# Kernel optimization log

Hardware: AMD Instinct MI355X
Metric: run time of the kernel (lower is better)

## Reference

```python
import jax, jax.numpy as jnp
import numpy as np

EMBED = 1024
NUM_EXPERTS = 8
TOP_K = 2


def setup_inputs() -> dict:
    key = jax.random.key(0)
    ks = jax.random.split(key, 6)
    scale = EMBED ** -0.5  # keep activations numerically sane
    return {
        "x": jax.random.normal(ks[0], (4, 4096, EMBED), jnp.float32),
        "router_w": jax.random.normal(ks[1], (EMBED, NUM_EXPERTS), jnp.float32) * scale,
        "router_b": jnp.zeros((NUM_EXPERTS,), jnp.float32),
        "we_gate": jax.random.normal(ks[2], (NUM_EXPERTS, EMBED, EMBED), jnp.float32) * scale,
        "we_up": jax.random.normal(ks[3], (NUM_EXPERTS, EMBED, EMBED), jnp.float32) * scale,
        "we_down": jax.random.normal(ks[4], (NUM_EXPERTS, EMBED, EMBED), jnp.float32) * scale,
    }


def reference(x, router_w, router_b, we_gate, we_up, we_down):
    x_shape = x.shape
    x_flat = x.reshape(-1, x_shape[-1])            # [T, D]
    num_tokens = x_flat.shape[0]

    router_logits = x_flat @ router_w + router_b    # [T, E]
    topk_weights, topk_indices = jax.lax.top_k(router_logits, k=TOP_K)
    topk_weights = jax.nn.softmax(topk_weights, axis=-1)  # [T, K]

    token_idx_mesh = jnp.repeat(jnp.arange(num_tokens), TOP_K)  # [T*K]
    expert_idx_mesh = topk_indices.reshape(-1)                  # [T*K]

    sort_permutation = jnp.argsort(expert_idx_mesh)  # stable sort by expert
    sorted_expert_idx = expert_idx_mesh[sort_permutation]
    sorted_token_idx = token_idx_mesh[sort_permutation]
    group_sizes = jnp.bincount(sorted_expert_idx, length=NUM_EXPERTS)

    sorted_tokens = x_flat[sorted_token_idx]  # [T*K, D] gather (ragged dispatch)

    ff_gate = jax.lax.ragged_dot(sorted_tokens, we_gate, group_sizes)  # [T*K, D]
    ff_up = jax.lax.ragged_dot(sorted_tokens, we_up, group_sizes)      # [T*K, D]
    activated = jax.nn.silu(ff_gate) * ff_up
    ff_out = jax.lax.ragged_dot(activated, we_down, group_sizes)       # [T*K, D]

    # fuse router weighting into the combine (scatter-add) step
    sorted_weights = topk_weights.reshape(-1)[sort_permutation]  # [T*K]
    ff_out = ff_out * sorted_weights[:, None]

    output_flat = jnp.zeros_like(x_flat).at[sorted_token_idx].add(ff_out)
    return output_flat.reshape(x_shape)
```

## Files before the change

### kernel.cpp

```cpp
#include <hip/hip_runtime.h>
#include <hip/hip_bf16.h>
#include <cstdint>
#include <cstddef>

typedef unsigned short u16;
typedef unsigned int u32;
typedef __attribute__((ext_vector_type(8))) short short8;
typedef __attribute__((ext_vector_type(4))) float floatx4;

#define DD 1024
#define NE 8

#define GLOAD_LDS16(G, L)                                               \
  __builtin_amdgcn_global_load_lds(                                     \
      (const __attribute__((address_space(1))) void*)(G),               \
      (__attribute__((address_space(3))) void*)(L), 16, 0, 0)

__device__ __forceinline__ u16 f2bf(float f) {
  union { __hip_bfloat16 h; u16 u; } cv;
  cv.h = __float2bfloat16(f);
  return cv.u;
}

__device__ __forceinline__ float2 bf2f2(u32 u) {
  union { u32 v; float f; } lo, hi;
  lo.v = u << 16; hi.v = u & 0xffff0000u;
  float2 r; r.x = lo.f; r.y = hi.f; return r;
}

__global__ __launch_bounds__(256) void router_kernel(
    const float* __restrict__ x, const float* __restrict__ rw,
    const float* __restrict__ rb, int2* __restrict__ experts,
    float2* __restrict__ wts, u16* __restrict__ xbf, int T) {
  const int wave = threadIdx.x >> 6;
  const int lane = threadIdx.x & 63;
  const int t = blockIdx.x * 4 + wave;
  if (t >= T) return;
  const float* xr = x + (size_t)t * DD;
  float acc[NE] = {0.f, 0.f, 0.f, 0.f, 0.f, 0.f, 0.f, 0.f};
#pragma unroll
  for (int i = 0; i < 16; i++) {
    const int idx = lane + i * 64;
    const float xv = xr[idx];
    xbf[(size_t)t * DD + idx] = f2bf(xv);
    const float4* r4 = (const float4*)(rw + (size_t)idx * NE);
    float4 a = r4[0], b = r4[1];
    acc[0] += xv * a.x; acc[1] += xv * a.y; acc[2] += xv * a.z; acc[3] += xv * a.w;
    acc[4] += xv * b.x; acc[5] += xv * b.y; acc[6] += xv * b.z; acc[7] += xv * b.w;
  }
#pragma unroll
  for (int s = 1; s < 64; s <<= 1)
#pragma unroll
    for (int e = 0; e < NE; e++)
      acc[e] += __shfl_xor(acc[e], s);
  if (lane == 0) {
    float lg[NE];
#pragma unroll
    for (int e = 0; e < NE; e++) lg[e] = acc[e] + rb[e];
    float l0 = lg[0]; int i0 = 0;
#pragma unroll
    for (int e = 1; e < NE; e++) if (lg[e] > l0) { l0 = lg[e]; i0 = e; }
    float l1 = -3.4e38f; int i1 = 0;
#pragma unroll
    for (int e = 0; e < NE; e++) {
      if (e == i0) continue;
      if (lg[e] > l1) { l1 = lg[e]; i1 = e; }
    }
    const float w0 = 1.f / (1.f + expf(l1 - l0));
    experts[t] = make_int2(i0, i1);
    wts[t] = make_float2(w0, 1.f - w0);
  }
}

__global__ __launch_bounds__(256) void count_kernel(
    const int2* __restrict__ experts, int* __restrict__ counts, int T) {
  __shared__ int lc[NE];
  if (threadIdx.x < NE) lc[threadIdx.x] = 0;
  __syncthreads();
  const int t = blockIdx.x * 256 + threadIdx.x;
  if (t < T) {
    int2 e = experts[t];
    atomicAdd(&lc[e.x], 1);
    atomicAdd(&lc[e.y], 1);
  }
  __syncthreads();
  if (threadIdx.x < NE && lc[threadIdx.x] > 0)
    atomicAdd(&counts[threadIdx.x], lc[threadIdx.x]);
}

__global__ void offsets_kernel(const int* __restrict__ counts, int* __restrict__ offsets) {
  int s = 0;
  for (int e = 0; e < NE; e++) { offsets[e] = s; s += counts[e]; }
}

__global__ __launch_bounds__(256) void scatter_kernel(
    const int2* __restrict__ experts, const int* __restrict__ offsets,
    int* __restrict__ cursors, int* __restrict__ tok_id,
    int2* __restrict__ slots, int T) {
  __shared__ int lc[NE], lb[NE];
  if (threadIdx.x < NE) lc[threadIdx.x] = 0;
  __syncthreads();
  const int t = blockIdx.x * 256 + threadIdx.x;
  int2 e = make_int2(0, 0);
  int p0 = 0, p1 = 0;
  if (t < T) {
    e = experts[t];
    p0 = atomicAdd(&lc[e.x], 1);
    p1 = atomicAdd(&lc[e.y], 1);
  }
  __syncthreads();
  if (threadIdx.x < NE) lb[threadIdx.x] = atomicAdd(&cursors[threadIdx.x], lc[threadIdx.x]);
  __syncthreads();
  if (t < T) {
    const int s0 = offsets[e.x] + lb[e.x] + p0;
    const int s1 = offsets[e.y] + lb[e.y] + p1;
    tok_id[s0] = t;
    tok_id[s1] = t;
    slots[t] = make_int2(s0, s1);
  }
}

__global__ __launch_bounds__(256) void convert_kernel(
    const float* __restrict__ wg, const float* __restrict__ wu,
    const float* __restrict__ wd, u16* __restrict__ Wgu, u16* __restrict__ Wd) {
  const int z = blockIdx.z;
  const int mat = z >> 3;
  const int e = z & 7;
  const float* src = (mat == 0 ? wg : (mat == 1 ? wu : wd)) + (size_t)e * DD * DD;
  __shared__ float tile[64][65];
  const int k0 = blockIdx.y * 64, n0 = blockIdx.x * 64;
  const int tx = threadIdx.x & 63, ty = threadIdx.x >> 6;
#pragma unroll
  for (int i = 0; i < 16; i++) {
    const int kk = i * 4 + ty;
    tile[kk][tx] = src[(size_t)(k0 + kk) * DD + n0 + tx];
  }
  __syncthreads();
#pragma unroll
  for (int i = 0; i < 16; i++) {
    const int nn = i * 4 + ty;
    const int n = n0 + nn;
    const u16 h = f2bf(tile[tx][nn]);
    if (mat == 2) {
      Wd[((size_t)e * DD + n) * DD + k0 + tx] = h;
    } else {
      const int nc = ((n >> 3) << 4) | (mat << 3) | (n & 7);
      Wgu[((size_t)e * 2048 + nc) * DD + k0 + tx] = h;
    }
  }
}

__global__ __launch_bounds__(256) void gateup_kernel(
    const u16* __restrict__ xbf, const u16* __restrict__ Wgu,
    const int* __restrict__ tok_id, const int* __restrict__ offsets,
    const int* __restrict__ counts, u16* __restrict__ H) {
  const int e = blockIdx.z;
  const int cnt = counts[e];
  const int m0 = blockIdx.y * 128;
  if (m0 >= cnt) return;
  const int off = offsets[e];
  const int n0 = blockIdx.x * 128;

  __shared__ u16 As[128 * 64];
  __shared__ u16 Bs[128 * 64];

  const int t = threadIdx.x;
  const int lane = t & 63;
  const int wave = t >> 6;
  const int wm = (wave >> 1) * 64;
  const int wn = (wave & 1) * 64;
  const int r16 = lane & 15;
  const int quad = lane >> 4;

  const int drow = t >> 3;
  const int dpos = t & 7;
  const u16* srcA[4];
  const u16* srcB[4];
  const u16* bbase = Wgu + ((size_t)e * 2048 + n0) * DD;
#pragma unroll
  for (int i = 0; i < 4; i++) {
    const int row = drow + i * 32;
    int r = m0 + row; if (r > cnt - 1) r = cnt - 1;
    const int tok = tok_id[off + r];
    const int ka = (dpos ^ (row & 7)) * 8;
    srcA[i] = xbf + (size_t)tok * DD + ka;
    srcB[i] = bbase + (size_t)row * DD + ka;
  }

  floatx4 acc[4][4];
#pragma unroll
  for (int i = 0; i < 4; i++)
#pragma unroll
    for (int j = 0; j < 4; j++)
      acc[i][j] = (floatx4){0.f, 0.f, 0.f, 0.f};

#pragma unroll 1
  for (int k0 = 0; k0 < DD; k0 += 64) {
    __syncthreads();
#pragma unroll
    for (int i = 0; i < 4; i++) {
      GLOAD_LDS16(srcA[i] + k0, &As[t * 8 + i * 2048]);
      GLOAD_LDS16(srcB[i] + k0, &Bs[t * 8 + i * 2048]);
    }
    __syncthreads();
#pragma unroll
    for (int s = 0; s < 2; s++) {
      short8 a[4], b[4];
#pragma unroll
      for (int i = 0; i < 4; i++)
        a[i] = *(const short8*)&As[(wm + i * 16 + r16) * 64 + (((s << 2) + quad) ^ (r16 & 7)) * 8];
#pragma unroll
      for (int j = 0; j < 4; j++)
        b[j] = *(const short8*)&Bs[(wn + j * 16 + r16) * 64 + (((s << 2) + quad) ^ (r16 & 7)) * 8];
#pragma unroll
      for (int i = 0; i < 4; i++)
#pragma unroll
        for (int j = 0; j < 4; j++)
          acc[i][j] = __builtin_amdgcn_mfma_f32_16x16x32_bf16(a[i], b[j], acc[i][j], 0, 0, 0);
    }
  }

#pragma unroll
  for (int i = 0; i < 4; i++) {
    const int mb = m0 + wm + i * 16 + quad * 4;
#pragma unroll
    for (int j = 0; j < 4; j++) {
      const int nc = n0 + wn + j * 16 + r16;
      const int ng = ((nc >> 4) << 3) | (nc & 7);
#pragma unroll
      for (int r = 0; r < 4; r++) {
        const float v = acc[i][j][r];
        const float pv = __shfl_xor(v, 8);
        const float g = (lane & 8) ? pv : v;
        const float u = (lane & 8) ? v : pv;
        const float hv = g * u / (1.f + __expf(-g));
        const int m = mb + r;
        if (!(lane & 8) && m < cnt)
          H[(size_t)(off + m) * DD + ng] = f2bf(hv);
      }
    }
  }
}

__global__ __launch_bounds__(256) void down_kernel(
    const u16* __restrict__ H, const u16* __restrict__ Wd,
    const int* __restrict__ counts, const int* __restrict__ offsets,
    u16* __restrict__ Y, int TK2) {
  const int e = blockIdx.z;
  const int cnt = counts[e];
  const int m0 = blockIdx.y * 128;
  if (m0 >= cnt) return;
  const int off = offsets[e];
  const int n0 = blockIdx.x * 128;

  __shared__ u16 As[128 * 64];
  __shared__ u16 Bs[128 * 64];

  const int t = threadIdx.x;
  const int lane = t & 63;
  const int wave = t >> 6;
  const int wm = (wave >> 1) * 64;
  const int wn = (wave & 1) * 64;
  const int r16 = lane & 15;
  const int quad = lane >> 4;

  const int drow = t >> 3;
  const int dpos = t & 7;
  const u16* srcA[4];
  const u16* srcB[4];
  const u16* bbase = Wd + ((size_t)e * DD + n0) * DD;
#pragma unroll
  for (int i = 0; i < 4; i++) {
    const int row = drow + i * 32;
    int r = off + m0 + row; if (r > TK2 - 1) r = TK2 - 1;
    const int ka = (dpos ^ (row & 7)) * 8;
    srcA[i] = H + (size_t)r * DD + ka;
    srcB[i] = bbase + (size_t)row * DD + ka;
  }

  floatx4 acc[4][4];
#pragma unroll
  for (int i = 0; i < 4; i++)
#pragma unroll
    for (int j = 0; j < 4; j++)
      acc[i][j] = (floatx4){0.f, 0.f, 0.f, 0.f};

#pragma unroll 1
  for (int k0 = 0; k0 < DD; k0 += 64) {
    __syncthreads();
#pragma unroll
    for (int i = 0; i < 4; i++) {
      GLOAD_LDS16(srcA[i] + k0, &As[t * 8 + i * 2048]);
      GLOAD_LDS16(srcB[i] + k0, &Bs[t * 8 + i * 2048]);
    }
    __syncthreads();
#pragma unroll
    for (int s = 0; s < 2; s++) {
      short8 a[4], b[4];
#pragma unroll
      for (int i = 0; i < 4; i++)
        a[i] = *(const short8*)&As[(wm + i * 16 + r16) * 64 + (((s << 2) + quad) ^ (r16 & 7)) * 8];
#pragma unroll
      for (int j = 0; j < 4; j++)
        b[j] = *(const short8*)&Bs[(wn + j * 16 + r16) * 64 + (((s << 2) + quad) ^ (r16 & 7)) * 8];
#pragma unroll
      for (int i = 0; i < 4; i++)
#pragma unroll
        for (int j = 0; j < 4; j++)
          acc[i][j] = __builtin_amdgcn_mfma_f32_16x16x32_bf16(a[i], b[j], acc[i][j], 0, 0, 0);
    }
  }

#pragma unroll
  for (int i = 0; i < 4; i++) {
    const int mb = m0 + wm + i * 16 + quad * 4;
#pragma unroll
    for (int r = 0; r < 4; r++) {
      const int m = mb + r;
      if (m < cnt) {
        u16* yrow = Y + (size_t)(off + m) * DD + n0 + wn + r16;
#pragma unroll
        for (int j = 0; j < 4; j++)
          yrow[j * 16] = f2bf(acc[i][j][r]);
      }
    }
  }
}

__global__ __launch_bounds__(256) void combine_kernel(
    const u16* __restrict__ Y, const int2* __restrict__ slots,
    const float2* __restrict__ wts, float* __restrict__ out, int T) {
  const int wave = threadIdx.x >> 6;
  const int lane = threadIdx.x & 63;
  const int t = blockIdx.x * 4 + wave;
  if (t >= T) return;
  const int2 s = slots[t];
  const float2 w = wts[t];
  const uint4* y0 = (const uint4*)(Y + (size_t)s.x * DD);
  const uint4* y1 = (const uint4*)(Y + (size_t)s.y * DD);
  float4* o = (float4*)(out + (size_t)t * DD);
#pragma unroll
  for (int c = 0; c < 2; c++) {
    const int idx = lane + c * 64;
    const uint4 a = y0[idx];
    const uint4 b = y1[idx];
    const u32 au[4] = {a.x, a.y, a.z, a.w};
    const u32 bu[4] = {b.x, b.y, b.z, b.w};
    float4 r[2];
#pragma unroll
    for (int q = 0; q < 4; q++) {
      const float2 fa = bf2f2(au[q]);
      const float2 fb = bf2f2(bu[q]);
      ((float*)r)[q * 2]     = w.x * fa.x + w.y * fb.x;
      ((float*)r)[q * 2 + 1] = w.x * fa.y + w.y * fb.y;
    }
    o[idx * 2]     = r[0];
    o[idx * 2 + 1] = r[1];
  }
}

extern "C" void kernel_launch(void* const* d_in, const int* in_sizes, int n_in,
                              void* d_out, int out_size, void* d_ws, size_t ws_size,
                              hipStream_t stream) {
  const float* x  = (const float*)d_in[0];
  const float* rw = (const float*)d_in[1];
  const float* rb = (const float*)d_in[2];
  const float* wg = (const float*)d_in[3];
  const float* wu = (const float*)d_in[4];
  const float* wd = (const float*)d_in[5];
  float* out = (float*)d_out;
  const int T = in_sizes[0] / DD;
  const int TK2 = 2 * T;

  char* p = (char*)d_ws;
  int* ctrl = (int*)p; p += 256;
  int2* experts = (int2*)p;  p += (size_t)T * 8;
  float2* wtsp  = (float2*)p; p += (size_t)T * 8;
  int* tok_id   = (int*)p;   p += (size_t)TK2 * 4;
  int2* slots   = (int2*)p;  p += (size_t)T * 8;
  u16* Wd       = (u16*)p;   p += (size_t)NE * DD * DD * 2;
  u16* H        = (u16*)p;   p += (size_t)TK2 * DD * 2;
  u16* Wgu      = (u16*)p;
  u16* xbf      = (u16*)(p + (size_t)NE * 2048 * DD * 2);
  u16* Y        = (u16*)p;
  p += (size_t)TK2 * DD * 2;
  if ((size_t)(p - (char*)d_ws) > ws_size) return;

  hipMemsetAsync(ctrl, 0, 256, stream);

  router_kernel<<<T / 4, 256, 0, stream>>>(x, rw, rb, experts, wtsp, xbf, T);
  count_kernel<<<T / 256, 256, 0, stream>>>(experts, ctrl, T);
  offsets_kernel<<<1, 1, 0, stream>>>(ctrl, ctrl + 16);
  scatter_kernel<<<T / 256, 256, 0, stream>>>(experts, ctrl + 16, ctrl + 8, tok_id, slots, T);
  convert_kernel<<<dim3(16, 16, 24), 256, 0, stream>>>(wg, wu, wd, Wgu, Wd);
  gateup_kernel<<<dim3(16, (T + 127) / 128, NE), 256, 0, stream>>>(
      xbf, Wgu, tok_id, ctrl + 16, ctrl, H);
  down_kernel<<<dim3(8, (T + 127) / 128, NE), 256, 0, stream>>>(
      H, Wd, ctrl, ctrl + 16, Y, TK2);
  combine_kernel<<<T / 4, 256, 0, stream>>>(Y, slots, wtsp, out, T);
}
```

Before: 517.5 us.

## Use 256x256 tiles with 4-stage async LDS pipeline in expert GEMMs

Both expert GEMM kernels move from 128x128 tiles with 256 threads and a single-buffered K=64 loop to 256x256 tiles with 512 threads. They now use a 4-deep ring of K=32 LDS buffers filled by direct global-to-LDS loads, gated with explicit vmcnt waits and raw barriers. MFMA sections are wrapped in s_setprio, and the LDS swizzle is reworked for the 32-wide rows. The aim is to overlap global loads with MFMA work and raise arithmetic intensity per block. The cost is 128 KB of LDS per block, 128 accumulator registers per lane, and more wasted work on ragged expert tails.

Measured after the change: 587.9 us. 13.6% more time.

```diff
diff --git a/kernel.cpp b/kernel.cpp
--- a/kernel.cpp
+++ b/kernel.cpp
@@ -150,78 +150,105 @@
   }
 }
 
-__global__ __launch_bounds__(256) void gateup_kernel(
+
+#define GEMM256_LOOP()                                                  \
+  STAGE(0); STAGE(1); STAGE(2);                                         \
+  asm volatile("s_waitcnt vmcnt(8)" ::: "memory");                      \
+  __builtin_amdgcn_s_barrier();                                         \
+  asm volatile("" ::: "memory");                                        \
+  _Pragma("unroll 1")                                                   \
+  for (int kt = 0; kt < 29; ++kt) {                                     \
+    STAGE((kt + 3) & 3);                                                \
+    COMPUTE((kt & 3) * 8192);                                           \
+    asm volatile("s_waitcnt vmcnt(8)" ::: "memory");                    \
+    __builtin_amdgcn_s_barrier();                                       \
+    asm volatile("" ::: "memory");                                      \
+  }                                                                     \
+  COMPUTE(1 * 8192);                                                    \
+  asm volatile("s_waitcnt vmcnt(4)" ::: "memory");                      \
+  __builtin_amdgcn_s_barrier();                                         \
+  asm volatile("" ::: "memory");                                        \
+  COMPUTE(2 * 8192);                                                    \
+  asm volatile("s_waitcnt vmcnt(0)" ::: "memory");                      \
+  __builtin_amdgcn_s_barrier();                                         \
+  asm volatile("" ::: "memory");                                        \
+  COMPUTE(3 * 8192);
+
+#define STAGE(BUF)                                                      \
+  {                                                                     \
+    GLOAD_LDS16(sA0, &As[(BUF) * 8192 + t * 8]);                        \
+    GLOAD_LDS16(sA1, &As[(BUF) * 8192 + 4096 + t * 8]);                 \
+    GLOAD_LDS16(sB0, &Bs[(BUF) * 8192 + t * 8]);                        \
+    GLOAD_LDS16(sB1, &Bs[(BUF) * 8192 + 4096 + t * 8]);                 \
+    sA0 += 32; sA1 += 32; sB0 += 32; sB1 += 32;                         \
+  }
+
+#define COMPUTE(BUFO)                                                   \
+  {                                                                     \
+    short8 a[8], b[4];                                                  \
+    _Pragma("unroll")                                                   \
+    for (int i = 0; i < 8; i++)                                         \
+      a[i] = *(const short8*)&As[(BUFO) + offA + i * 512];              \
+    _Pragma("unroll")                                                   \
+    for (int j = 0; j < 4; j++)                                         \
+      b[j] = *(const short8*)&Bs[(BUFO) + offB + j * 512];              \
+    __builtin_amdgcn_s_setprio(1);                                      \
+    _Pragma("unroll")                                                   \
+    for (int i = 0; i < 8; i++)                                         \
+      _Pragma("unroll")                                                 \
+      for (int j = 0; j < 4; j++)                                       \
+        acc[i][j] = __builtin_amdgcn_mfma_f32_16x16x32_bf16(            \
+            a[i], b[j], acc[i][j], 0, 0, 0);                            \
+    __builtin_amdgcn_s_setprio(0);                                      \
+  }
+
+__global__ __launch_bounds__(512, 2) void gateup_kernel(
     const u16* __restrict__ xbf, const u16* __restrict__ Wgu,
     const int* __restrict__ tok_id, const int* __restrict__ offsets,
     const int* __restrict__ counts, u16* __restrict__ H) {
   const int e = blockIdx.z;
   const int cnt = counts[e];
-  const int m0 = blockIdx.y * 128;
+  const int m0 = blockIdx.y * 256;
   if (m0 >= cnt) return;
   const int off = offsets[e];
-  const int n0 = blockIdx.x * 128;
-
-  __shared__ u16 As[128 * 64];
-  __shared__ u16 Bs[128 * 64];
+  const int n0 = blockIdx.x * 256;
+
+  __shared__ u16 As[4 * 8192];
+  __shared__ u16 Bs[4 * 8192];
 
   const int t = threadIdx.x;
   const int lane = t & 63;
   const int wave = t >> 6;
-  const int wm = (wave >> 1) * 64;
-  const int wn = (wave & 1) * 64;
+  const int wm = (wave >> 2) * 128;
+  const int wn = (wave & 3) * 64;
   const int r16 = lane & 15;
   const int quad = lane >> 4;
-
-  const int drow = t >> 3;
-  const int dpos = t & 7;
-  const u16* srcA[4];
-  const u16* srcB[4];
-  const u16* bbase = Wgu + ((size_t)e * 2048 + n0) * DD;
-#pragma unroll
-  for (int i = 0; i < 4; i++) {
-    const int row = drow + i * 32;
-    int r = m0 + row; if (r > cnt - 1) r = cnt - 1;
-    const int tok = tok_id[off + r];
-    const int ka = (dpos ^ (row & 7)) * 8;
-    srcA[i] = xbf + (size_t)tok * DD + ka;
-    srcB[i] = bbase + (size_t)row * DD + ka;
-  }
-
-  floatx4 acc[4][4];
-#pragma unroll
-  for (int i = 0; i < 4; i++)
+  const int swz = quad ^ ((r16 >> 1) & 3);
+  const int offA = (wm + r16) * 32 + swz * 8;
+  const int offB = (wn + r16) * 32 + swz * 8;
+
+  const int drow = t >> 2;
+  const int dpos = t & 3;
+  const int c8 = (dpos ^ ((drow >> 1) & 3)) * 8;
+  int r0 = m0 + drow;       if (r0 > cnt - 1) r0 = cnt - 1;
+  int r1 = m0 + drow + 128; if (r1 > cnt - 1) r1 = cnt - 1;
+  const u16* sA0 = xbf + (size_t)tok_id[off + r0] * DD + c8;
+  const u16* sA1 = xbf + (size_t)tok_id[off + r1] * DD + c8;
+  const u16* bbase = Wgu + ((size_t)e * 2048 + n0) * DD + c8;
+  const u16* sB0 = bbase + (size_t)drow * DD;
+  const u16* sB1 = bbase + (size_t)(drow + 128) * DD;
+
+  floatx4 acc[8][4];
+#pragma unroll
+  for (int i = 0; i < 8; i++)
 #pragma unroll
     for (int j = 0; j < 4; j++)
       acc[i][j] = (floatx4){0.f, 0.f, 0.f, 0.f};
 
-#pragma unroll 1
-  for (int k0 = 0; k0 < DD; k0 += 64) {
-    __syncthreads();
-#pragma unroll
-    for (int i = 0; i < 4; i++) {
-      GLOAD_LDS16(srcA[i] + k0, &As[t * 8 + i * 2048]);
-      GLOAD_LDS16(srcB[i] + k0, &Bs[t * 8 + i * 2048]);
-    }
-    __syncthreads();
-#pragma unroll
-    for (int s = 0; s < 2; s++) {
-      short8 a[4], b[4];
-#pragma unroll
-      for (int i = 0; i < 4; i++)
-        a[i] = *(const short8*)&As[(wm + i * 16 + r16) * 64 + (((s << 2) + quad) ^ (r16 & 7)) * 8];
-#pragma unroll
-      for (int j = 0; j < 4; j++)
-        b[j] = *(const short8*)&Bs[(wn + j * 16 + r16) * 64 + (((s << 2) + quad) ^ (r16 & 7)) * 8];
-#pragma unroll
-      for (int i = 0; i < 4; i++)
-#pragma unroll
-        for (int j = 0; j < 4; j++)
-          acc[i][j] = __builtin_amdgcn_mfma_f32_16x16x32_bf16(a[i], b[j], acc[i][j], 0, 0, 0);
-    }
-  }
-
-#pragma unroll
-  for (int i = 0; i < 4; i++) {
+  GEMM256_LOOP();
+
+#pragma unroll
+  for (int i = 0; i < 8; i++) {
     const int mb = m0 + wm + i * 16 + quad * 4;
 #pragma unroll
     for (int j = 0; j < 4; j++) {
@@ -242,77 +269,53 @@
   }
 }
 
-__global__ __launch_bounds__(256) void down_kernel(
+__global__ __launch_bounds__(512, 2) void down_kernel(
     const u16* __restrict__ H, const u16* __restrict__ Wd,
     const int* __restrict__ counts, const int* __restrict__ offsets,
     u16* __restrict__ Y, int TK2) {
   const int e = blockIdx.z;
   const int cnt = counts[e];
-  const int m0 = blockIdx.y * 128;
+  const int m0 = blockIdx.y * 256;
   if (m0 >= cnt) return;
   const int off = offsets[e];
-  const int n0 = blockIdx.x * 128;
-
-  __shared__ u16 As[128 * 64];
-  __shared__ u16 Bs[128 * 64];
+  const int n0 = blockIdx.x * 256;
+
+  __shared__ u16 As[4 * 8192];
+  __shared__ u16 Bs[4 * 8192];
 
   const int t = threadIdx.x;
   const int lane = t & 63;
   const int wave = t >> 6;
-  const int wm = (wave >> 1) * 64;
-  const int wn = (wave & 1) * 64;
+  const int wm = (wave >> 2) * 128;
+  const int wn = (wave & 3) * 64;
   const int r16 = lane & 15;
   const int quad = lane >> 4;
-
-  const int drow = t >> 3;
-  const int dpos = t & 7;
-  const u16* srcA[4];
-  const u16* srcB[4];
-  const u16* bbase = Wd + ((size_t)e * DD + n0) * DD;
-#pragma unroll
-  for (int i = 0; i < 4; i++) {
-    const int row = drow + i * 32;
-    int r = off + m0 + row; if (r > TK2 - 1) r = TK2 - 1;
-    const int ka = (dpos ^ (row & 7)) * 8;
-    srcA[i] = H + (size_t)r * DD + ka;
-    srcB[i] = bbase + (size_t)row * DD + ka;
-  }
-
-  floatx4 acc[4][4];
-#pragma unroll
-  for (int i = 0; i < 4; i++)
+  const int swz = quad ^ ((r16 >> 1) & 3);
+  const int offA = (wm + r16) * 32 + swz * 8;
+  const int offB = (wn + r16) * 32 + swz * 8;
+
+  const int drow = t >> 2;
+  const int dpos = t & 3;
+  const int c8 = (dpos ^ ((drow >> 1) & 3)) * 8;
+  int r0 = off + m0 + drow;       if (r0 > TK2 - 1) r0 = TK2 - 1;
+  int r1 = off + m0 + drow + 128; if (r1 > TK2 - 1) r1 = TK2 - 1;
+  const u16* sA0 = H + (size_t)r0 * DD + c8;
+  const u16* sA1 = H + (size_t)r1 * DD + c8;
+  const u16* bbase = Wd + ((size_t)e * DD + n0) * DD + c8;
+  const u16* sB0 = bbase + (size_t)drow * DD;
+  const u16* sB1 = bbase + (size_t)(drow + 128) * DD;
+
+  floatx4 acc[8][4];
+#pragma unroll
+  for (int i = 0; i < 8; i++)
 #pragma unroll
     for (int j = 0; j < 4; j++)
       acc[i][j] = (floatx4){0.f, 0.f, 0.f, 0.f};
 
-#pragma unroll 1
-  for (int k0 = 0; k0 < DD; k0 += 64) {
-    __syncthreads();
-#pragma unroll
-    for (int i = 0; i < 4; i++) {
-      GLOAD_LDS16(srcA[i] + k0, &As[t * 8 + i * 2048]);
-      GLOAD_LDS16(srcB[i] + k0, &Bs[t * 8 + i * 2048]);
-    }
-    __syncthreads();
-#pragma unroll
-    for (int s = 0; s < 2; s++) {
-      short8 a[4], b[4];
-#pragma unroll
-      for (int i = 0; i < 4; i++)
-        a[i] = *(const short8*)&As[(wm + i * 16 + r16) * 64 + (((s << 2) + quad) ^ (r16 & 7)) * 8];
-#pragma unroll
-      for (int j = 0; j < 4; j++)
-        b[j] = *(const short8*)&Bs[(wn + j * 16 + r16) * 64 + (((s << 2) + quad) ^ (r16 & 7)) * 8];
-#pragma unroll
-      for (int i = 0; i < 4; i++)
-#pragma unroll
-        for (int j = 0; j < 4; j++)
-          acc[i][j] = __builtin_amdgcn_mfma_f32_16x16x32_bf16(a[i], b[j], acc[i][j], 0, 0, 0);
-    }
-  }
-
-#pragma unroll
-  for (int i = 0; i < 4; i++) {
+  GEMM256_LOOP();
+
+#pragma unroll
+  for (int i = 0; i < 8; i++) {
     const int mb = m0 + wm + i * 16 + quad * 4;
 #pragma unroll
     for (int r = 0; r < 4; r++) {
@@ -326,6 +329,9 @@
     }
   }
 }
+
+#undef STAGE
+#undef COMPUTE
 
 __global__ __launch_bounds__(256) void combine_kernel(
     const u16* __restrict__ Y, const int2* __restrict__ slots,
@@ -393,9 +399,9 @@
   offsets_kernel<<<1, 1, 0, stream>>>(ctrl, ctrl + 16);
   scatter_kernel<<<T / 256, 256, 0, stream>>>(experts, ctrl + 16, ctrl + 8, tok_id, slots, T);
   convert_kernel<<<dim3(16, 16, 24), 256, 0, stream>>>(wg, wu, wd, Wgu, Wd);
-  gateup_kernel<<<dim3(16, (T + 127) / 128, NE), 256, 0, stream>>>(
+  gateup_kernel<<<dim3(8, (T + 255) / 256, NE), 512, 0, stream>>>(
       xbf, Wgu, tok_id, ctrl + 16, ctrl, H);
-  down_kernel<<<dim3(8, (T + 127) / 128, NE), 256, 0, stream>>>(
+  down_kernel<<<dim3(4, (T + 255) / 256, NE), 512, 0, stream>>>(
       H, Wd, ctrl, ctrl + 16, Y, TK2);
   combine_kernel<<<T / 4, 256, 0, stream>>>(Y, slots, wtsp, out, T);
 }
```

## Double-buffer LDS tiles in grouped GEMMs with inline-asm LDS reads and priority hints

Applied to the files above, without the earlier changes.

Both expert GEMM kernels now keep two LDS buffers, so the global-to-LDS copy for the next K tile is issued while MFMAs run on the current one, with one barrier per iteration instead of two. LDS fragment reads become hand-written ds_read_b128 with immediate offsets, wrapped in sched_barrier and s_setprio to keep the MFMA burst together. Launch bounds request two blocks per CU. LDS use per block doubles to 64KB, which may limit occupancy, and the manual waitcnt and scheduling fences give the compiler less freedom.

Result: slower. 529.2 us (+2.3%).

```diff
diff --git a/kernel.cpp b/kernel.cpp
--- a/kernel.cpp
+++ b/kernel.cpp
@@ -15,6 +15,11 @@
   __builtin_amdgcn_global_load_lds(                                     \
       (const __attribute__((address_space(1))) void*)(G),               \
       (__attribute__((address_space(3))) void*)(L), 16, 0, 0)
+
+#define LDSA(P) ((u32)(uintptr_t)(const __attribute__((address_space(3))) void*)(P))
+
+#define DSR(DST, ADDR, IMM)                                             \
+  asm volatile("ds_read_b128 %0, %1 offset:" IMM : "=v"(DST) : "v"(ADDR))
 
 __device__ __forceinline__ u16 f2bf(float f) {
   union { __hip_bfloat16 h; u16 u; } cv;
@@ -150,7 +155,61 @@
   }
 }
 
-__global__ __launch_bounds__(256) void gateup_kernel(
+
+#define STAGE(BUF, KOFF)                                                \
+  {                                                                     \
+    _Pragma("unroll")                                                   \
+    for (int i = 0; i < 4; i++) {                                       \
+      GLOAD_LDS16(srcA[i] + (KOFF), &As[(BUF) * 8192 + t * 8 + i * 2048]); \
+      GLOAD_LDS16(srcB[i] + (KOFF), &Bs[(BUF) * 8192 + t * 8 + i * 2048]); \
+    }                                                                   \
+  }
+
+#define COMPUTE(BUF)                                                    \
+  {                                                                     \
+    _Pragma("unroll")                                                   \
+    for (int s = 0; s < 2; s++) {                                       \
+      short8 a[4], b[4];                                                \
+      const u32 ab_ = asb + (u32)(BUF) * 16384u + offA + cks[s];        \
+      const u32 bb_ = bsb + (u32)(BUF) * 16384u + offB + cks[s];        \
+      DSR(a[0], ab_, "0");    DSR(a[1], ab_, "2048");                   \
+      DSR(a[2], ab_, "4096"); DSR(a[3], ab_, "6144");                   \
+      DSR(b[0], bb_, "0");    DSR(b[1], bb_, "2048");                   \
+      DSR(b[2], bb_, "4096"); DSR(b[3], bb_, "6144");                   \
+      asm volatile("s_waitcnt lgkmcnt(0)");                             \
+      __builtin_amdgcn_sched_barrier(0);                                \
+      __builtin_amdgcn_s_setprio(1);                                    \
+      _Pragma("unroll")                                                 \
+      for (int i = 0; i < 4; i++)                                       \
+        _Pragma("unroll")                                               \
+        for (int j = 0; j < 4; j++)                                     \
+          acc[i][j] = __builtin_amdgcn_mfma_f32_16x16x32_bf16(          \
+              a[i], b[j], acc[i][j], 0, 0, 0);                          \
+      __builtin_amdgcn_s_setprio(0);                                    \
+      __builtin_amdgcn_sched_barrier(0);                                \
+    }                                                                   \
+  }
+
+#define SYNC0()                                                         \
+  __builtin_amdgcn_sched_barrier(0);                                    \
+  asm volatile("s_waitcnt vmcnt(0)");                                   \
+  __builtin_amdgcn_s_barrier();                                         \
+  __builtin_amdgcn_sched_barrier(0);
+
+#define GEMM128_LOOP()                                                  \
+  STAGE(0, 0);                                                          \
+  SYNC0();                                                              \
+  int cur = 0;                                                          \
+  _Pragma("unroll 1")                                                   \
+  for (int kk = 0; kk < 15; ++kk) {                                     \
+    STAGE(cur ^ 1, (kk + 1) * 64);                                      \
+    COMPUTE(cur);                                                       \
+    SYNC0();                                                            \
+    cur ^= 1;                                                           \
+  }                                                                     \
+  COMPUTE(cur);
+
+__global__ __launch_bounds__(256, 2) void gateup_kernel(
     const u16* __restrict__ xbf, const u16* __restrict__ Wgu,
     const int* __restrict__ tok_id, const int* __restrict__ offsets,
     const int* __restrict__ counts, u16* __restrict__ H) {
@@ -161,8 +220,8 @@
   const int off = offsets[e];
   const int n0 = blockIdx.x * 128;
 
-  __shared__ u16 As[128 * 64];
-  __shared__ u16 Bs[128 * 64];
+  __shared__ u16 As[2 * 8192];
+  __shared__ u16 Bs[2 * 8192];
 
   const int t = threadIdx.x;
   const int lane = t & 63;
@@ -171,6 +230,13 @@
   const int wn = (wave & 1) * 64;
   const int r16 = lane & 15;
   const int quad = lane >> 4;
+  const u32 offA = (u32)((wm + r16) * 128);
+  const u32 offB = (u32)((wn + r16) * 128);
+  u32 cks[2];
+  cks[0] = (u32)(((quad) ^ (r16 & 7)) * 16);
+  cks[1] = (u32)(((4 + quad) ^ (r16 & 7)) * 16);
+  const u32 asb = LDSA(&As[0]);
+  const u32 bsb = LDSA(&Bs[0]);
 
   const int drow = t >> 3;
   const int dpos = t & 7;
@@ -194,31 +260,7 @@
     for (int j = 0; j < 4; j++)
       acc[i][j] = (floatx4){0.f, 0.f, 0.f, 0.f};
 
-#pragma unroll 1
-  for (int k0 = 0; k0 < DD; k0 += 64) {
-    __syncthreads();
-#pragma unroll
-    for (int i = 0; i < 4; i++) {
-      GLOAD_LDS16(srcA[i] + k0, &As[t * 8 + i * 2048]);
-      GLOAD_LDS16(srcB[i] + k0, &Bs[t * 8 + i * 2048]);
-    }
-    __syncthreads();
-#pragma unroll
-    for (int s = 0; s < 2; s++) {
-      short8 a[4], b[4];
-#pragma unroll
-      for (int i = 0; i < 4; i++)
-        a[i] = *(const short8*)&As[(wm + i * 16 + r16) * 64 + (((s << 2) + quad) ^ (r16 & 7)) * 8];
-#pragma unroll
-      for (int j = 0; j < 4; j++)
-        b[j] = *(const short8*)&Bs[(wn + j * 16 + r16) * 64 + (((s << 2) + quad) ^ (r16 & 7)) * 8];
-#pragma unroll
-      for (int i = 0; i < 4; i++)
-#pragma unroll
-        for (int j = 0; j < 4; j++)
-          acc[i][j] = __builtin_amdgcn_mfma_f32_16x16x32_bf16(a[i], b[j], acc[i][j], 0, 0, 0);
-    }
-  }
+  GEMM128_LOOP();
 
 #pragma unroll
   for (int i = 0; i < 4; i++) {
@@ -242,7 +284,7 @@
   }
 }
 
-__global__ __launch_bounds__(256) void down_kernel(
+__global__ __launch_bounds__(256, 2) void down_kernel(
     const u16* __restrict__ H, const u16* __restrict__ Wd,
     const int* __restrict__ counts, const int* __restrict__ offsets,
     u16* __restrict__ Y, int TK2) {
@@ -253,8 +295,8 @@
   const int off = offsets[e];
   const int n0 = blockIdx.x * 128;
 
-  __shared__ u16 As[128 * 64];
-  __shared__ u16 Bs[128 * 64];
+  __shared__ u16 As[2 * 8192];
+  __shared__ u16 Bs[2 * 8192];
 
   const int t = threadIdx.x;
   const int lane = t & 63;
@@ -263,6 +305,13 @@
   const int wn = (wave & 1) * 64;
   const int r16 = lane & 15;
   const int quad = lane >> 4;
+  const u32 offA = (u32)((wm + r16) * 128);
+  const u32 offB = (u32)((wn + r16) * 128);
+  u32 cks[2];
+  cks[0] = (u32)(((quad) ^ (r16 & 7)) * 16);
+  cks[1] = (u32)(((4 + quad) ^ (r16 & 7)) * 16);
+  const u32 asb = LDSA(&As[0]);
+  const u32 bsb = LDSA(&Bs[0]);
 
   const int drow = t >> 3;
   const int dpos = t & 7;
@@ -285,31 +334,7 @@
     for (int j = 0; j < 4; j++)
       acc[i][j] = (floatx4){0.f, 0.f, 0.f, 0.f};
 
-#pragma unroll 1
-  for (int k0 = 0; k0 < DD; k0 += 64) {
-    __syncthreads();
-#pragma unroll
-    for (int i = 0; i < 4; i++) {
-      GLOAD_LDS16(srcA[i] + k0, &As[t * 8 + i * 2048]);
-      GLOAD_LDS16(srcB[i] + k0, &Bs[t * 8 + i * 2048]);
-    }
-    __syncthreads();
-#pragma unroll
-    for (int s = 0; s < 2; s++) {
-      short8 a[4], b[4];
-#pragma unroll
-      for (int i = 0; i < 4; i++)
-        a[i] = *(const short8*)&As[(wm + i * 16 + r16) * 64 + (((s << 2) + quad) ^ (r16 & 7)) * 8];
-#pragma unroll
-      for (int j = 0; j < 4; j++)
-        b[j] = *(const short8*)&Bs[(wn + j * 16 + r16) * 64 + (((s << 2) + quad) ^ (r16 & 7)) * 8];
-#pragma unroll
-      for (int i = 0; i < 4; i++)
-#pragma unroll
-        for (int j = 0; j < 4; j++)
-          acc[i][j] = __builtin_amdgcn_mfma_f32_16x16x32_bf16(a[i], b[j], acc[i][j], 0, 0, 0);
-    }
-  }
+  GEMM128_LOOP();
 
 #pragma unroll
   for (int i = 0; i < 4; i++) {
@@ -326,6 +351,10 @@
     }
   }
 }
+
+#undef STAGE
+#undef COMPUTE
+#undef SYNC0
 
 __global__ __launch_bounds__(256) void combine_kernel(
     const u16* __restrict__ Y, const int2* __restrict__ slots,
```
